# Kernel tuning notes

Hardware: AMD Instinct MI355X
Metric: run time of the kernel (lower is better)

The kernel has to match this reference:

```python
import jax, jax.numpy as jnp
import numpy as np

B, L, D, H = 4, 2048, 1024, 16
HD = D // H  # head_dim = 64


def setup_inputs() -> dict:
    key = jax.random.key(0)
    ks = jax.random.split(key, 13)
    s = 1.0 / np.sqrt(D)
    inp = {
        'q': jax.random.normal(ks[0], (B, L, D), jnp.float32),
        'k': jax.random.normal(ks[1], (B, L, D), jnp.float32),
        'v': jax.random.normal(ks[2], (B, L, D), jnp.float32),
        'mask': jax.random.randint(ks[3], (B, 1, L, L), 0, 2, jnp.int32),
        'WQ': jax.random.normal(ks[4], (D, D), jnp.float32) * s,
        'bQ': jnp.zeros((D,), jnp.float32),
        'WK': jax.random.normal(ks[5], (D, D), jnp.float32) * s,
        'bK': jnp.zeros((D,), jnp.float32),
        'WV': jax.random.normal(ks[6], (D, D), jnp.float32) * s,
        'bV': jnp.zeros((D,), jnp.float32),
        'WO': jax.random.normal(ks[7], (D, D), jnp.float32) * s,
        'bO': jnp.zeros((D,), jnp.float32),
    }
    return inp


def reference(q, k, v, mask, WQ, bQ, WK, bK, WV, bV, WO, bO):
    # Linear projections (torch Linear: x @ W.T + b; here W stored as [D,D], use x @ W + b equivalently)
    Q = q @ WQ + bQ  # [B, L, D]
    K = k @ WK + bK
    V = v @ WV + bV
    # split heads -> [B, H, L, HD]
    Q = Q.reshape(B, L, H, HD).transpose(0, 2, 1, 3)
    K = K.reshape(B, L, H, HD).transpose(0, 2, 1, 3)
    V = V.reshape(B, L, H, HD).transpose(0, 2, 1, 3)
    scale = 1.0 / np.sqrt(HD).astype(np.float32)
    scores = jnp.einsum('bhqd,bhkd->bhqk', Q, K) * scale  # [B, H, Lq, Lk]
    scores = jnp.where(mask == 0, -jnp.inf, scores)  # mask broadcasts over heads
    attn = jax.nn.softmax(scores, axis=-1)
    # dropout p=0 (eval) -> identity
    ctx = jnp.einsum('bhqk,bhkd->bhqd', attn, V)  # [B, H, L, HD]
    ctx = ctx.transpose(0, 2, 1, 3).reshape(B, L, D)
    return ctx @ WO + bO
```

## Files before the change

### kernel.cpp

```cpp
#include <hip/hip_runtime.h>
#include <math.h>

#define B_  4
#define L_  2048
#define D_  1024
#define H_  16
#define HD_ 64

typedef __attribute__((ext_vector_type(8))) short short8;
typedef __attribute__((ext_vector_type(4))) float f32x4;

__device__ static inline unsigned short f2bf(float f) {
    union { float f; unsigned int u; } v; v.f = f;
    const unsigned int u = v.u;
    return (unsigned short)((u + 0x7FFFu + ((u >> 16) & 1u)) >> 16);
}

__device__ static inline unsigned cvt_pk_bf16(float a, float b) {
    unsigned r;
    asm("v_cvt_pk_bf16_f32 %0, %1, %2" : "=v"(r) : "v"(a), "v"(b));
    return r;
}

__device__ static inline void async_copy16(const void* g, void* lds)
{
    __builtin_amdgcn_global_load_lds(
        (const __attribute__((address_space(1))) void*)g,
        (__attribute__((address_space(3))) void*)lds, 16, 0, 0);
}

__global__ __launch_bounds__(256) void cvt_bf16_kernel(
    const float* __restrict__ in, unsigned short* __restrict__ out)
{
    const size_t i = ((size_t)blockIdx.x * 256 + threadIdx.x) * 8;
    const float4 x = *(const float4*)&in[i];
    const float4 y = *(const float4*)&in[i + 4];
    ushort4 o0, o1;
    o0.x = f2bf(x.x); o0.y = f2bf(x.y); o0.z = f2bf(x.z); o0.w = f2bf(x.w);
    o1.x = f2bf(y.x); o1.y = f2bf(y.y); o1.z = f2bf(y.z); o1.w = f2bf(y.w);
    *(ushort4*)&out[i]     = o0;
    *(ushort4*)&out[i + 4] = o1;
}

__global__ __launch_bounds__(256) void transpose_bf16_kernel(
    const float* __restrict__ W, unsigned short* __restrict__ WT)
{
    __shared__ float t[32][33];
    const int c  = threadIdx.x & 31;
    const int r8 = threadIdx.x >> 5;
    const int k0 = blockIdx.y * 32;
    const int n0 = blockIdx.x * 32;
    #pragma unroll
    for (int i = 0; i < 4; ++i) {
        const int r = r8 + i * 8;
        t[r][c] = W[(size_t)(k0 + r) * 1024 + n0 + c];
    }
    __syncthreads();
    #pragma unroll
    for (int i = 0; i < 4; ++i) {
        const int r = r8 + i * 8;
        WT[(size_t)(n0 + r) * 1024 + k0 + c] = f2bf(t[c][r]);
    }
}

__global__ __launch_bounds__(256) void vtrans_bf16_kernel(
    const unsigned short* __restrict__ Vb, unsigned short* __restrict__ vtb)
{
    __shared__ unsigned short t[64][68];
    const int tid = threadIdx.x;
    const int l0  = blockIdx.x * 64;
    const int h   = blockIdx.y;
    const int b   = blockIdx.z;
    const int rr  = tid >> 4;
    const int c4  = (tid & 15) * 4;
    #pragma unroll
    for (int i = 0; i < 4; ++i) {
        const int r = i * 16 + rr;
        *(ushort4*)&t[r][c4] =
            *(const ushort4*)&Vb[((size_t)(b * L_ + l0 + r)) * D_ + h * 64 + c4];
    }
    __syncthreads();
    #pragma unroll
    for (int i = 0; i < 4; ++i) {
        const int d = i * 16 + rr;
        ushort4 o;
        o.x = t[c4 + 0][d]; o.y = t[c4 + 1][d];
        o.z = t[c4 + 2][d]; o.w = t[c4 + 3][d];
        *(ushort4*)&vtb[((size_t)((b * H_ + h) * 64 + d)) * L_ + l0 + c4] = o;
    }
}

__global__ __launch_bounds__(256) void pack_mask16_kernel(
    const int* __restrict__ mask, unsigned short* __restrict__ mbt)
{
    const unsigned g = blockIdx.x * 256 + threadIdx.x;
    const int v = mask[g];
    const unsigned long long bm = __ballot(v != 0);
    const int lane = threadIdx.x & 63;
    if (lane < 4) {
        const int b  = g >> 22;
        const int q  = (g >> 11) & 2047;
        const int kt = (g >> 6) & 31;
        unsigned long long x = (bm >> (4 * lane)) & 0x000F000F000F000FULL;
        x |= x >> 12;
        x |= x >> 24;
        mbt[((size_t)(b * 32 + kt) * 2048 + q) * 4 + lane] =
            (unsigned short)(x & 0xFFFFu);
    }
}

template<int OUT_BF16>
__global__ __launch_bounds__(256) void gemm_mfma_kernel(
    const unsigned short* __restrict__ A, const unsigned short* __restrict__ WT,
    const float* __restrict__ bias, void* __restrict__ Cv,
    int M, int N, int K, float omul)
{
    __shared__ __align__(16) unsigned short At[128 * 64];
    __shared__ __align__(16) unsigned short Bt[128 * 64];

    const int tid  = threadIdx.x;
    const int lane = tid & 63;
    const int wave = tid >> 6;
    const int wm   = wave >> 1;
    const int wn   = wave & 1;
    const int quad = lane >> 4;
    const int l15  = lane & 15;
    const int m0   = blockIdx.y * 128;
    const int n0   = blockIdx.x * 128;

    f32x4 acc[4][4];
    #pragma unroll
    for (int i = 0; i < 4; ++i)
        #pragma unroll
        for (int j = 0; j < 4; ++j) acc[i][j] = (f32x4)0.f;

    for (int k0 = 0; k0 < K; k0 += 64) {
        __syncthreads();
        #pragma unroll
        for (int i = 0; i < 4; ++i) {
            const int fb  = i * 256 + wave * 64;
            const int f   = fb + lane;
            const int row = f >> 3;
            const int c8  = f & 7;
            async_copy16(&A [(size_t)(m0 + row) * K + k0 + c8 * 8],
                         (char*)At + (size_t)fb * 16);
            async_copy16(&WT[(size_t)(n0 + row) * K + k0 + c8 * 8],
                         (char*)Bt + (size_t)fb * 16);
        }
        __syncthreads();

        #pragma unroll
        for (int kk = 0; kk < 64; kk += 32) {
            short8 afr[4], bfr[4];
            #pragma unroll
            for (int mt = 0; mt < 4; ++mt)
                afr[mt] = *(const short8*)&At[(size_t)(wm * 64 + mt * 16 + l15) * 64 + kk + quad * 8];
            #pragma unroll
            for (int nt = 0; nt < 4; ++nt)
                bfr[nt] = *(const short8*)&Bt[(size_t)(wn * 64 + nt * 16 + l15) * 64 + kk + quad * 8];
            #pragma unroll
            for (int mt = 0; mt < 4; ++mt)
                #pragma unroll
                for (int nt = 0; nt < 4; ++nt)
                    acc[mt][nt] = __builtin_amdgcn_mfma_f32_16x16x32_bf16(
                        afr[mt], bfr[nt], acc[mt][nt], 0, 0, 0);
        }
    }

    #pragma unroll
    for (int nt = 0; nt < 4; ++nt) {
        const int col = n0 + wn * 64 + nt * 16 + l15;
        const float bv = bias[col];
        #pragma unroll
        for (int mt = 0; mt < 4; ++mt) {
            const int r0 = m0 + wm * 64 + mt * 16 + quad * 4;
            #pragma unroll
            for (int r = 0; r < 4; ++r) {
                const float val = (acc[mt][nt][r] + bv) * omul;
                if constexpr (OUT_BF16)
                    ((unsigned short*)Cv)[(size_t)(r0 + r) * N + col] = f2bf(val);
                else
                    ((float*)Cv)[(size_t)(r0 + r) * N + col] = val;
            }
        }
    }
}

#define AQ 128
#define AK 64
#define PSTR 72

__global__ __launch_bounds__(256) void attn_mfma_kernel(
    const unsigned short* __restrict__ Qb,
    const unsigned short* __restrict__ Kb,
    const unsigned short* __restrict__ Vtg,
    const unsigned short* __restrict__ mbt,
    unsigned short* __restrict__ Cb)
{
    __shared__ __align__(16) unsigned short Kt[AK * 64];
    __shared__ __align__(16) unsigned short Vs[64 * AK];
    __shared__ __align__(16) unsigned short Pt[AQ * PSTR];
    __shared__ __align__(16) unsigned short Mt[AQ * 4];

    const int tid  = threadIdx.x;
    const int lane = tid & 63;
    const int w    = tid >> 6;
    const int quad = lane >> 4;
    const int l15  = lane & 15;
    const int q0   = blockIdx.x * AQ;
    const int h    = blockIdx.y;
    const int b    = blockIdx.z;

    short8 qf[2][2];
    #pragma unroll
    for (int qc = 0; qc < 2; ++qc)
        #pragma unroll
        for (int kc = 0; kc < 2; ++kc)
            qf[qc][kc] = *(const short8*)
                &Qb[((size_t)(b * L_ + q0 + w * 32 + qc * 16 + l15)) * D_
                    + h * 64 + kc * 32 + quad * 8];

    f32x4 ot[4][2];
    #pragma unroll
    for (int dr = 0; dr < 4; ++dr)
        #pragma unroll
        for (int qc = 0; qc < 2; ++qc) ot[dr][qc] = (f32x4)0.f;
    float m_run[2] = {-INFINITY, -INFINITY};
    float l_run[2] = {0.f, 0.f};

    for (int kt = 0; kt < L_ / AK; ++kt) {
        const int k0 = kt * AK;
        __syncthreads();
        #pragma unroll
        for (int i = 0; i < 2; ++i) {
            const int fb = i * 256 + w * 64;
            const int f  = fb + lane;
            const int r  = f >> 3;
            const int cs = (f & 7) ^ (r & 7);
            async_copy16(&Kb[((size_t)(b * L_ + k0 + r)) * D_ + h * 64 + cs * 8],
                         (char*)Kt + fb * 16);
            async_copy16(&Vtg[((size_t)((b * H_ + h) * 64 + r)) * L_ + k0 + cs * 8],
                         (char*)Vs + fb * 16);
        }
        if (w == 3)
            async_copy16(&mbt[((size_t)(b * 32 + kt) * 2048 + q0) * 4 + lane * 8],
                         (char*)Mt);
        __syncthreads();

        f32x4 st[4][2];
        {
            short8 kf[4];
            #pragma unroll
            for (int kr = 0; kr < 4; ++kr)
                kf[kr] = *(const short8*)
                    &Kt[(kr * 16 + l15) * 64 + ((quad ^ (l15 & 7)) * 8)];
            #pragma unroll
            for (int kr = 0; kr < 4; ++kr)
                #pragma unroll
                for (int qc = 0; qc < 2; ++qc)
                    st[kr][qc] = __builtin_amdgcn_mfma_f32_16x16x32_bf16(
                        kf[kr], qf[qc][0], (f32x4)0.f, 0, 0, 0);
        }
        {
            short8 kf[4];
            #pragma unroll
            for (int kr = 0; kr < 4; ++kr)
                kf[kr] = *(const short8*)
                    &Kt[(kr * 16 + l15) * 64 + (((4 + quad) ^ (l15 & 7)) * 8)];
            #pragma unroll
            for (int kr = 0; kr < 4; ++kr)
                #pragma unroll
                for (int qc = 0; qc < 2; ++qc)
                    st[kr][qc] = __builtin_amdgcn_mfma_f32_16x16x32_bf16(
                        kf[kr], qf[qc][1], st[kr][qc], 0, 0, 0);
        }

        #pragma unroll
        for (int qc = 0; qc < 2; ++qc) {
            const unsigned m16 = Mt[(w * 32 + qc * 16 + l15) * 4 + quad];
            float rmax = -INFINITY;
            #pragma unroll
            for (int kr = 0; kr < 4; ++kr) {
                const unsigned nib = (m16 >> (kr * 4)) & 0xFu;
                #pragma unroll
                for (int r = 0; r < 4; ++r) {
                    const float x = ((nib >> r) & 1u) ? st[kr][qc][r] : -INFINITY;
                    st[kr][qc][r] = x;
                    rmax = fmaxf(rmax, x);
                }
            }
            rmax = fmaxf(rmax, __shfl_xor(rmax, 16));
            rmax = fmaxf(rmax, __shfl_xor(rmax, 32));
            if (__any(rmax > m_run[qc] + 8.f)) {
                const float mnew  = fmaxf(m_run[qc], rmax);
                const float msafe = fmaxf(mnew, -1e30f);
                const float alpha = exp2f(m_run[qc] - msafe);
                l_run[qc] *= alpha;
                #pragma unroll
                for (int dr = 0; dr < 4; ++dr) {
                    ot[dr][qc][0] *= alpha; ot[dr][qc][1] *= alpha;
                    ot[dr][qc][2] *= alpha; ot[dr][qc][3] *= alpha;
                }
                m_run[qc] = mnew;
            }
            const float msafe = fmaxf(m_run[qc], -1e30f);
            float psum = 0.f;
            #pragma unroll
            for (int kr = 0; kr < 4; ++kr) {
                const float p0 = exp2f(st[kr][qc][0] - msafe);
                const float p1 = exp2f(st[kr][qc][1] - msafe);
                const float p2 = exp2f(st[kr][qc][2] - msafe);
                const float p3 = exp2f(st[kr][qc][3] - msafe);
                psum += (p0 + p1) + (p2 + p3);
                uint2 pk;
                pk.x = cvt_pk_bf16(p0, p1);
                pk.y = cvt_pk_bf16(p2, p3);
                *(uint2*)&Pt[(w * 32 + qc * 16 + l15) * PSTR + kr * 16 + quad * 4] = pk;
            }
            psum += __shfl_xor(psum, 16);
            psum += __shfl_xor(psum, 32);
            l_run[qc] += psum;
        }

        #pragma unroll
        for (int kc = 0; kc < 2; ++kc) {
            short8 vf[4], pf[2];
            #pragma unroll
            for (int dr = 0; dr < 4; ++dr)
                vf[dr] = *(const short8*)
                    &Vs[(dr * 16 + l15) * 64 + (((kc * 4 + quad) ^ (l15 & 7)) * 8)];
            #pragma unroll
            for (int qc = 0; qc < 2; ++qc)
                pf[qc] = *(const short8*)&Pt[(w * 32 + qc * 16 + l15) * PSTR
                                             + kc * 32 + quad * 8];
            #pragma unroll
            for (int dr = 0; dr < 4; ++dr)
                #pragma unroll
                for (int qc = 0; qc < 2; ++qc)
                    ot[dr][qc] = __builtin_amdgcn_mfma_f32_16x16x32_bf16(
                        vf[dr], pf[qc], ot[dr][qc], 0, 0, 0);
        }
    }

    #pragma unroll
    for (int qc = 0; qc < 2; ++qc) {
        const float rinv = (l_run[qc] > 0.f) ? (1.f / l_run[qc]) : 0.f;
        const size_t base = ((size_t)(b * L_ + q0 + w * 32 + qc * 16 + l15)) * D_
                            + h * 64;
        #pragma unroll
        for (int dr = 0; dr < 4; ++dr) {
            ushort4 o;
            o.x = f2bf(ot[dr][qc][0] * rinv);
            o.y = f2bf(ot[dr][qc][1] * rinv);
            o.z = f2bf(ot[dr][qc][2] * rinv);
            o.w = f2bf(ot[dr][qc][3] * rinv);
            *(ushort4*)&Cb[base + dr * 16 + quad * 4] = o;
        }
    }
}

extern "C" void kernel_launch(void* const* d_in, const int* in_sizes, int n_in,
                              void* d_out, int out_size, void* d_ws, size_t ws_size,
                              hipStream_t stream)
{
    const float* q    = (const float*)d_in[0];
    const float* k    = (const float*)d_in[1];
    const float* v    = (const float*)d_in[2];
    const int*   mask = (const int*)d_in[3];
    const float* WQ   = (const float*)d_in[4];
    const float* bQ   = (const float*)d_in[5];
    const float* WK   = (const float*)d_in[6];
    const float* bK   = (const float*)d_in[7];
    const float* WV   = (const float*)d_in[8];
    const float* bV   = (const float*)d_in[9];
    const float* WO   = (const float*)d_in[10];
    const float* bO   = (const float*)d_in[11];
    float* out = (float*)d_out;

    const size_t NTOK = (size_t)B_ * L_;

    char* W = (char*)d_ws;
    unsigned short* qin = (unsigned short*)(W);
    unsigned short* kin = (unsigned short*)(W + ((size_t)16  << 20));
    unsigned short* vin = (unsigned short*)(W + ((size_t)32  << 20));
    unsigned short* qbf = (unsigned short*)(W + ((size_t)48  << 20));
    unsigned short* kbf = (unsigned short*)(W + ((size_t)64  << 20));
    unsigned short* vbf = (unsigned short*)(W + ((size_t)80  << 20));
    unsigned short* vtb = (unsigned short*)(W + ((size_t)96  << 20));
    unsigned short* cb  = (unsigned short*)(W + ((size_t)112 << 20));
    unsigned short* WTo = vin;

    unsigned short* mbt16 = (unsigned short*)d_out;
    unsigned short* WTq = (unsigned short*)((char*)d_out + ((size_t)2 << 20));
    unsigned short* WTk = (unsigned short*)((char*)d_out + ((size_t)4 << 20));
    unsigned short* WTv = (unsigned short*)((char*)d_out + ((size_t)6 << 20));

    pack_mask16_kernel<<<(B_ * L_ * L_) / 256, 256, 0, stream>>>(mask, mbt16);

    const int cvtg = (int)(NTOK * D_ / (256 * 8));
    cvt_bf16_kernel<<<cvtg, 256, 0, stream>>>(q, qin);
    cvt_bf16_kernel<<<cvtg, 256, 0, stream>>>(k, kin);
    cvt_bf16_kernel<<<cvtg, 256, 0, stream>>>(v, vin);

    dim3 tg(32, 32);
    transpose_bf16_kernel<<<tg, 256, 0, stream>>>(WQ, WTq);
    transpose_bf16_kernel<<<tg, 256, 0, stream>>>(WK, WTk);
    transpose_bf16_kernel<<<tg, 256, 0, stream>>>(WV, WTv);

    const float qscale = 0.125f * 1.44269504088896340736f;
    dim3 ggrd(D_ / 128, NTOK / 128);
    gemm_mfma_kernel<1><<<ggrd, 256, 0, stream>>>(qin, WTq, bQ, qbf, (int)NTOK, D_, D_, qscale);
    gemm_mfma_kernel<1><<<ggrd, 256, 0, stream>>>(kin, WTk, bK, kbf, (int)NTOK, D_, D_, 1.f);
    gemm_mfma_kernel<1><<<ggrd, 256, 0, stream>>>(vin, WTv, bV, vbf, (int)NTOK, D_, D_, 1.f);

    transpose_bf16_kernel<<<tg, 256, 0, stream>>>(WO, WTo);
    vtrans_bf16_kernel<<<dim3(L_ / 64, H_, B_), 256, 0, stream>>>(vbf, vtb);

    dim3 agrd(L_ / AQ, H_, B_);
    attn_mfma_kernel<<<agrd, 256, 0, stream>>>(qbf, kbf, vtb, mbt16, cb);

    gemm_mfma_kernel<0><<<ggrd, 256, 0, stream>>>(cb, WTo, bO, out, (int)NTOK, D_, D_, 1.f);
}
```

Before: 533.9 us.

## Batch QKV launches, double-buffer attention tiles, remap blocks, raise MFMA priority

Merges the three input conversions, three weight transposes and three QKV projection GEMMs into single launches indexed by a grid dimension. The attention kernel now double-buffers its K, V and mask tiles in LDS, so the next tile loads while the current one is computed. It also uses a 1-D grid with a remapped block order so that blocks sharing a batch and head are spread across the XCDs. s_setprio hints are placed around the MFMA sections. Together these aim to cut launch overhead and hide attention load latency, at the cost of more LDS per block, which may reduce occupancy.

Measured after the change: 509.1 us. 1.05x faster.

```diff
diff --git a/kernel.cpp b/kernel.cpp
--- a/kernel.cpp
+++ b/kernel.cpp
@@ -29,23 +29,54 @@
         (__attribute__((address_space(3))) void*)lds, 16, 0, 0);
 }
 
-__global__ __launch_bounds__(256) void cvt_bf16_kernel(
-    const float* __restrict__ in, unsigned short* __restrict__ out)
-{
+__global__ __launch_bounds__(256) void cvt3_bf16_kernel(
+    const float* __restrict__ i0, const float* __restrict__ i1,
+    const float* __restrict__ i2,
+    unsigned short* __restrict__ o0, unsigned short* __restrict__ o1,
+    unsigned short* __restrict__ o2)
+{
+    const float* in = blockIdx.y == 0 ? i0 : blockIdx.y == 1 ? i1 : i2;
+    unsigned short* out = blockIdx.y == 0 ? o0 : blockIdx.y == 1 ? o1 : o2;
     const size_t i = ((size_t)blockIdx.x * 256 + threadIdx.x) * 8;
     const float4 x = *(const float4*)&in[i];
     const float4 y = *(const float4*)&in[i + 4];
-    ushort4 o0, o1;
-    o0.x = f2bf(x.x); o0.y = f2bf(x.y); o0.z = f2bf(x.z); o0.w = f2bf(x.w);
-    o1.x = f2bf(y.x); o1.y = f2bf(y.y); o1.z = f2bf(y.z); o1.w = f2bf(y.w);
-    *(ushort4*)&out[i]     = o0;
-    *(ushort4*)&out[i + 4] = o1;
+    ushort4 a0, a1;
+    a0.x = f2bf(x.x); a0.y = f2bf(x.y); a0.z = f2bf(x.z); a0.w = f2bf(x.w);
+    a1.x = f2bf(y.x); a1.y = f2bf(y.y); a1.z = f2bf(y.z); a1.w = f2bf(y.w);
+    *(ushort4*)&out[i]     = a0;
+    *(ushort4*)&out[i + 4] = a1;
 }
 
 __global__ __launch_bounds__(256) void transpose_bf16_kernel(
     const float* __restrict__ W, unsigned short* __restrict__ WT)
 {
     __shared__ float t[32][33];
+    const int c  = threadIdx.x & 31;
+    const int r8 = threadIdx.x >> 5;
+    const int k0 = blockIdx.y * 32;
+    const int n0 = blockIdx.x * 32;
+    #pragma unroll
+    for (int i = 0; i < 4; ++i) {
+        const int r = r8 + i * 8;
+        t[r][c] = W[(size_t)(k0 + r) * 1024 + n0 + c];
+    }
+    __syncthreads();
+    #pragma unroll
+    for (int i = 0; i < 4; ++i) {
+        const int r = r8 + i * 8;
+        WT[(size_t)(n0 + r) * 1024 + k0 + c] = f2bf(t[c][r]);
+    }
+}
+
+__global__ __launch_bounds__(256) void trans3_bf16_kernel(
+    const float* __restrict__ W0, const float* __restrict__ W1,
+    const float* __restrict__ W2,
+    unsigned short* __restrict__ T0, unsigned short* __restrict__ T1,
+    unsigned short* __restrict__ T2)
+{
+    __shared__ float t[32][33];
+    const float* W = blockIdx.z == 0 ? W0 : blockIdx.z == 1 ? W1 : W2;
+    unsigned short* WT = blockIdx.z == 0 ? T0 : blockIdx.z == 1 ? T1 : T2;
     const int c  = threadIdx.x & 31;
     const int r8 = threadIdx.x >> 5;
     const int k0 = blockIdx.y * 32;
@@ -110,14 +141,12 @@
 }
 
 template<int OUT_BF16>
-__global__ __launch_bounds__(256) void gemm_mfma_kernel(
+__device__ static inline void gemm_body(
     const unsigned short* __restrict__ A, const unsigned short* __restrict__ WT,
     const float* __restrict__ bias, void* __restrict__ Cv,
-    int M, int N, int K, float omul)
-{
-    __shared__ __align__(16) unsigned short At[128 * 64];
-    __shared__ __align__(16) unsigned short Bt[128 * 64];
-
+    int M, int N, int K, float omul,
+    unsigned short* At, unsigned short* Bt)
+{
     const int tid  = threadIdx.x;
     const int lane = tid & 63;
     const int wave = tid >> 6;
@@ -158,12 +187,14 @@
             #pragma unroll
             for (int nt = 0; nt < 4; ++nt)
                 bfr[nt] = *(const short8*)&Bt[(size_t)(wn * 64 + nt * 16 + l15) * 64 + kk + quad * 8];
+            __builtin_amdgcn_s_setprio(1);
             #pragma unroll
             for (int mt = 0; mt < 4; ++mt)
                 #pragma unroll
                 for (int nt = 0; nt < 4; ++nt)
                     acc[mt][nt] = __builtin_amdgcn_mfma_f32_16x16x32_bf16(
                         afr[mt], bfr[nt], acc[mt][nt], 0, 0, 0);
+            __builtin_amdgcn_s_setprio(0);
         }
     }
 
@@ -186,9 +217,41 @@
     }
 }
 
+__global__ __launch_bounds__(256) void gemm3_mfma_kernel(
+    const unsigned short* __restrict__ A0, const unsigned short* __restrict__ A1,
+    const unsigned short* __restrict__ A2,
+    const unsigned short* __restrict__ W0, const unsigned short* __restrict__ W1,
+    const unsigned short* __restrict__ W2,
+    const float* __restrict__ b0, const float* __restrict__ b1,
+    const float* __restrict__ b2,
+    unsigned short* __restrict__ C0, unsigned short* __restrict__ C1,
+    unsigned short* __restrict__ C2, float om0)
+{
+    __shared__ __align__(16) unsigned short At[128 * 64];
+    __shared__ __align__(16) unsigned short Bt[128 * 64];
+    const int z = blockIdx.z;
+    const unsigned short* A  = z == 0 ? A0 : z == 1 ? A1 : A2;
+    const unsigned short* WT = z == 0 ? W0 : z == 1 ? W1 : W2;
+    const float* bias        = z == 0 ? b0 : z == 1 ? b1 : b2;
+    unsigned short* C        = z == 0 ? C0 : z == 1 ? C1 : C2;
+    const float omul         = z == 0 ? om0 : 1.f;
+    gemm_body<1>(A, WT, bias, C, B_ * L_, D_, D_, omul, At, Bt);
+}
+
+__global__ __launch_bounds__(256) void gemm_mfma_kernel(
+    const unsigned short* __restrict__ A, const unsigned short* __restrict__ WT,
+    const float* __restrict__ bias, float* __restrict__ C,
+    int M, int N, int K)
+{
+    __shared__ __align__(16) unsigned short At[128 * 64];
+    __shared__ __align__(16) unsigned short Bt[128 * 64];
+    gemm_body<0>(A, WT, bias, C, M, N, K, 1.f, At, Bt);
+}
+
 #define AQ 128
 #define AK 64
 #define PSTR 72
+#define NT (L_ / AK)
 
 __global__ __launch_bounds__(256) void attn_mfma_kernel(
     const unsigned short* __restrict__ Qb,
@@ -197,19 +260,25 @@
     const unsigned short* __restrict__ mbt,
     unsigned short* __restrict__ Cb)
 {
-    __shared__ __align__(16) unsigned short Kt[AK * 64];
-    __shared__ __align__(16) unsigned short Vs[64 * AK];
+    __shared__ __align__(16) unsigned short Kt[2][AK * 64];
+    __shared__ __align__(16) unsigned short Vs[2][64 * AK];
     __shared__ __align__(16) unsigned short Pt[AQ * PSTR];
-    __shared__ __align__(16) unsigned short Mt[AQ * 4];
+    __shared__ __align__(16) unsigned short Mt[2][AQ * 4];
 
     const int tid  = threadIdx.x;
     const int lane = tid & 63;
     const int w    = tid >> 6;
     const int quad = lane >> 4;
     const int l15  = lane & 15;
-    const int q0   = blockIdx.x * AQ;
-    const int h    = blockIdx.y;
-    const int b    = blockIdx.z;
+
+    const int nid = (blockIdx.x & 7) * 128 + (blockIdx.x >> 3);
+    const int q0  = (nid & 15) * AQ;
+    const int h   = (nid >> 4) & 15;
+    const int b   = nid >> 8;
+
+    const unsigned short* kbase = &Kb [((size_t)(b * L_)) * D_ + h * 64];
+    const unsigned short* vbase = &Vtg[((size_t)((b * H_ + h) * 64)) * L_];
+    const unsigned short* mbase = &mbt[((size_t)(b * 32) * 2048 + q0) * 4];
 
     short8 qf[2][2];
     #pragma unroll
@@ -228,24 +297,30 @@
     float m_run[2] = {-INFINITY, -INFINITY};
     float l_run[2] = {0.f, 0.f};
 
-    for (int kt = 0; kt < L_ / AK; ++kt) {
+    auto stage = [&](int bi, int kt) {
         const int k0 = kt * AK;
-        __syncthreads();
         #pragma unroll
         for (int i = 0; i < 2; ++i) {
             const int fb = i * 256 + w * 64;
             const int f  = fb + lane;
             const int r  = f >> 3;
             const int cs = (f & 7) ^ (r & 7);
-            async_copy16(&Kb[((size_t)(b * L_ + k0 + r)) * D_ + h * 64 + cs * 8],
-                         (char*)Kt + fb * 16);
-            async_copy16(&Vtg[((size_t)((b * H_ + h) * 64 + r)) * L_ + k0 + cs * 8],
-                         (char*)Vs + fb * 16);
+            async_copy16(&kbase[(size_t)(k0 + r) * D_ + cs * 8],
+                         (char*)&Kt[bi][0] + fb * 16);
+            async_copy16(&vbase[(size_t)r * L_ + k0 + cs * 8],
+                         (char*)&Vs[bi][0] + fb * 16);
         }
         if (w == 3)
-            async_copy16(&mbt[((size_t)(b * 32 + kt) * 2048 + q0) * 4 + lane * 8],
-                         (char*)Mt);
-        __syncthreads();
+            async_copy16(&mbase[(size_t)kt * 2048 * 4 + lane * 8],
+                         (char*)&Mt[bi][0]);
+    };
+
+    stage(0, 0);
+    __syncthreads();
+
+    for (int kt = 0; kt < NT; ++kt) {
+        const int cur = kt & 1;
+        if (kt + 1 < NT) stage(cur ^ 1, kt + 1);
 
         f32x4 st[4][2];
         {
@@ -253,31 +328,35 @@
             #pragma unroll
             for (int kr = 0; kr < 4; ++kr)
                 kf[kr] = *(const short8*)
-                    &Kt[(kr * 16 + l15) * 64 + ((quad ^ (l15 & 7)) * 8)];
+                    &Kt[cur][(kr * 16 + l15) * 64 + ((quad ^ (l15 & 7)) * 8)];
+            __builtin_amdgcn_s_setprio(1);
             #pragma unroll
             for (int kr = 0; kr < 4; ++kr)
                 #pragma unroll
                 for (int qc = 0; qc < 2; ++qc)
                     st[kr][qc] = __builtin_amdgcn_mfma_f32_16x16x32_bf16(
                         kf[kr], qf[qc][0], (f32x4)0.f, 0, 0, 0);
+            __builtin_amdgcn_s_setprio(0);
         }
         {
             short8 kf[4];
             #pragma unroll
             for (int kr = 0; kr < 4; ++kr)
                 kf[kr] = *(const short8*)
-                    &Kt[(kr * 16 + l15) * 64 + (((4 + quad) ^ (l15 & 7)) * 8)];
+                    &Kt[cur][(kr * 16 + l15) * 64 + (((4 + quad) ^ (l15 & 7)) * 8)];
+            __builtin_amdgcn_s_setprio(1);
             #pragma unroll
             for (int kr = 0; kr < 4; ++kr)
                 #pragma unroll
                 for (int qc = 0; qc < 2; ++qc)
                     st[kr][qc] = __builtin_amdgcn_mfma_f32_16x16x32_bf16(
                         kf[kr], qf[qc][1], st[kr][qc], 0, 0, 0);
+            __builtin_amdgcn_s_setprio(0);
         }
 
         #pragma unroll
         for (int qc = 0; qc < 2; ++qc) {
-            const unsigned m16 = Mt[(w * 32 + qc * 16 + l15) * 4 + quad];
+            const unsigned m16 = Mt[cur][(w * 32 + qc * 16 + l15) * 4 + quad];
             float rmax = -INFINITY;
             #pragma unroll
             for (int kr = 0; kr < 4; ++kr) {
@@ -328,18 +407,22 @@
             #pragma unroll
             for (int dr = 0; dr < 4; ++dr)
                 vf[dr] = *(const short8*)
-                    &Vs[(dr * 16 + l15) * 64 + (((kc * 4 + quad) ^ (l15 & 7)) * 8)];
+                    &Vs[cur][(dr * 16 + l15) * 64 + (((kc * 4 + quad) ^ (l15 & 7)) * 8)];
             #pragma unroll
             for (int qc = 0; qc < 2; ++qc)
                 pf[qc] = *(const short8*)&Pt[(w * 32 + qc * 16 + l15) * PSTR
                                              + kc * 32 + quad * 8];
+            __builtin_amdgcn_s_setprio(1);
             #pragma unroll
             for (int dr = 0; dr < 4; ++dr)
                 #pragma unroll
                 for (int qc = 0; qc < 2; ++qc)
                     ot[dr][qc] = __builtin_amdgcn_mfma_f32_16x16x32_bf16(
                         vf[dr], pf[qc], ot[dr][qc], 0, 0, 0);
-        }
+            __builtin_amdgcn_s_setprio(0);
+        }
+
+        __syncthreads();
     }
 
     #pragma unroll
@@ -398,26 +481,21 @@
     pack_mask16_kernel<<<(B_ * L_ * L_) / 256, 256, 0, stream>>>(mask, mbt16);
 
     const int cvtg = (int)(NTOK * D_ / (256 * 8));
-    cvt_bf16_kernel<<<cvtg, 256, 0, stream>>>(q, qin);
-    cvt_bf16_kernel<<<cvtg, 256, 0, stream>>>(k, kin);
-    cvt_bf16_kernel<<<cvtg, 256, 0, stream>>>(v, vin);
-
-    dim3 tg(32, 32);
-    transpose_bf16_kernel<<<tg, 256, 0, stream>>>(WQ, WTq);
-    transpose_bf16_kernel<<<tg, 256, 0, stream>>>(WK, WTk);
-    transpose_bf16_kernel<<<tg, 256, 0, stream>>>(WV, WTv);
+    cvt3_bf16_kernel<<<dim3(cvtg, 3), 256, 0, stream>>>(q, k, v, qin, kin, vin);
+
+    trans3_bf16_kernel<<<dim3(32, 32, 3), 256, 0, stream>>>(
+        WQ, WK, WV, WTq, WTk, WTv);
 
     const float qscale = 0.125f * 1.44269504088896340736f;
+    dim3 ggrd3(D_ / 128, NTOK / 128, 3);
+    gemm3_mfma_kernel<<<ggrd3, 256, 0, stream>>>(
+        qin, kin, vin, WTq, WTk, WTv, bQ, bK, bV, qbf, kbf, vbf, qscale);
+
+    transpose_bf16_kernel<<<dim3(32, 32), 256, 0, stream>>>(WO, WTo);
+    vtrans_bf16_kernel<<<dim3(L_ / 64, H_, B_), 256, 0, stream>>>(vbf, vtb);
+
+    attn_mfma_kernel<<<dim3(1024), 256, 0, stream>>>(qbf, kbf, vtb, mbt16, cb);
+
     dim3 ggrd(D_ / 128, NTOK / 128);
-    gemm_mfma_kernel<1><<<ggrd, 256, 0, stream>>>(qin, WTq, bQ, qbf, (int)NTOK, D_, D_, qscale);
-    gemm_mfma_kernel<1><<<ggrd, 256, 0, stream>>>(kin, WTk, bK, kbf, (int)NTOK, D_, D_, 1.f);
-    gemm_mfma_kernel<1><<<ggrd, 256, 0, stream>>>(vin, WTv, bV, vbf, (int)NTOK, D_, D_, 1.f);
-
-    transpose_bf16_kernel<<<tg, 256, 0, stream>>>(WO, WTo);
-    vtrans_bf16_kernel<<<dim3(L_ / 64, H_, B_), 256, 0, stream>>>(vbf, vtb);
-
-    dim3 agrd(L_ / AQ, H_, B_);
-    attn_mfma_kernel<<<agrd, 256, 0, stream>>>(qbf, kbf, vtb, mbt16, cb);
-
-    gemm_mfma_kernel<0><<<ggrd, 256, 0, stream>>>(cb, WTo, bO, out, (int)NTOK, D_, D_, 1.f);
-}
+    gemm_mfma_kernel<<<ggrd, 256, 0, stream>>>(cb, WTo, bO, out, (int)NTOK, D_, D_);
+}
```
